# Optimization experiments

Hardware: AMD Instinct MI355X
Metric: run time of the kernel (lower is better)

The kernel has to match this reference:

```python
import jax, jax.numpy as jnp
import numpy as np

B, T, I, H, O = 128, 4096, 6, 32, 2


def setup_inputs() -> dict:
    key = jax.random.key(0)
    ks = jax.random.split(key, 8)
    x = jax.random.normal(ks[0], (B, T, I), dtype=jnp.float32)
    lengths = jax.random.randint(ks[1], (B,), 1, T + 1, dtype=jnp.int32)
    lengths = jnp.sort(lengths)[::-1]            # descending (enforce_sorted=True)
    lengths = lengths.at[0].set(T)               # max length == T -> static output shape
    s = 1.0 / np.sqrt(H)                         # PyTorch GRU/Linear init scale
    w_ih = jax.random.uniform(ks[2], (3 * H, I), minval=-s, maxval=s, dtype=jnp.float32)
    w_hh = jax.random.uniform(ks[3], (3 * H, H), minval=-s, maxval=s, dtype=jnp.float32)
    b_ih = jax.random.uniform(ks[4], (3 * H,), minval=-s, maxval=s, dtype=jnp.float32)
    b_hh = jax.random.uniform(ks[5], (3 * H,), minval=-s, maxval=s, dtype=jnp.float32)
    fc_w = jax.random.uniform(ks[6], (O, H), minval=-s, maxval=s, dtype=jnp.float32)
    fc_b = jax.random.uniform(ks[7], (O,), minval=-s, maxval=s, dtype=jnp.float32)
    return {"x": x, "lengths": lengths, "w_ih": w_ih, "w_hh": w_hh,
            "b_ih": b_ih, "b_hh": b_hh, "fc_w": fc_w, "fc_b": fc_b}


def reference(x, lengths, w_ih, w_hh, b_ih, b_hh, fc_w, fc_b):
    Bn, Tn, _ = x.shape
    Hn = w_hh.shape[1]
    # Precompute input-side gate projections for all steps (one big GEMM).
    gx = jnp.einsum('bti,gi->btg', x, w_ih) + b_ih      # [B,T,3H] (gate order: r,z,n)
    gx = jnp.swapaxes(gx, 0, 1)                          # [T,B,3H] time-major for scan
    mask = jnp.arange(Tn)[:, None] < lengths[None, :]    # [T,B] valid-step mask
    h0 = jnp.zeros((Bn, Hn), x.dtype)

    def step(h, inp):
        gxt, m = inp                                     # gxt [B,3H], m [B]
        gh = h @ w_hh.T + b_hh                           # [B,3H]
        xr, xz, xn = jnp.split(gxt, 3, axis=-1)
        hr, hz, hn = jnp.split(gh, 3, axis=-1)
        r = jax.nn.sigmoid(xr + hr)
        z = jax.nn.sigmoid(xz + hz)
        n = jnp.tanh(xn + r * hn)
        h_new = (1.0 - z) * n + z * h
        m = m[:, None]
        out = jnp.where(m, h_new, 0.0)                   # pad_packed pads with zeros
        h = jnp.where(m, h_new, h)                       # freeze state past length
        return h, out

    _, ys = jax.lax.scan(step, h0, (gx, mask))           # ys [T,B,H]
    out = jnp.swapaxes(ys, 0, 1)                         # [B,T,H]
    # fc applied to every (incl. zero-padded) timestep, as in the torch code
    return jnp.einsum('bth,oh->bto', out, fc_w) + fc_b   # [B,T,O]
```

## Files before the change

kernel.cpp:

```cpp
#include <hip/hip_runtime.h>

#define TT 4096
#define BB 128
#define L2E 1.4426950408889634f

typedef unsigned uv2 __attribute__((ext_vector_type(2)));
typedef float v2f __attribute__((ext_vector_type(2)));
typedef float v4f __attribute__((ext_vector_type(4)));
typedef __bf16 v8bf __attribute__((ext_vector_type(8)));

__device__ __forceinline__ float fexp2(float a) { return __builtin_amdgcn_exp2f(a); }

__device__ __forceinline__ float bpermf(int idx_bytes, float v) {
  return __int_as_float(__builtin_amdgcn_ds_bpermute(idx_bytes, __float_as_int(v)));
}

__device__ __forceinline__ float xhalf_sum(float p) {
#if __has_builtin(__builtin_amdgcn_permlane32_swap)
  uv2 r = __builtin_amdgcn_permlane32_swap(__float_as_uint(p), __float_as_uint(p),
                                           false, false);
  return __uint_as_float(r[0]) + __uint_as_float(r[1]);
#else
  return p + bpermf((threadIdx.x ^ 32) << 2, p);
#endif
}

__device__ __forceinline__ unsigned cvtpk(float lo, float hi) {
  unsigned r;
  asm("v_cvt_pk_bf16_f32 %0, %1, %2" : "=v"(r) : "v"(lo), "v"(hi));
  return r;
}

template <int CTRL>
__device__ __forceinline__ int dppmv(int src) {
  return __builtin_amdgcn_update_dpp(0, src, CTRL, 0xF, 0xF, true);
}

__device__ __forceinline__ v8bf frag_from(unsigned u0, unsigned u1, unsigned u2,
                                          unsigned u3) {
  uint4 uu = make_uint4(u0, u1, u2, u3);
  return __builtin_bit_cast(v8bf, uu);
}

__global__ __launch_bounds__(256) void gx_pre(
    const float* __restrict__ x, const float* __restrict__ w_ih,
    const float* __restrict__ b_ih, const float* __restrict__ b_hh,
    const int* __restrict__ lengths, float* __restrict__ gx) {
  const size_t idx = (size_t)blockIdx.x * 256 + threadIdx.x;
  const int g = (int)(idx % 96);
  const size_t bt = idx / 96;
  const int b = (int)(bt >> 12);
  const int t = (int)(bt & (TT - 1));
  if (t >= lengths[b]) return;
  const float* xp = x + bt * 6;
  float acc = (g < 64) ? (b_ih[g] + b_hh[g]) : b_ih[g];
#pragma unroll
  for (int i = 0; i < 6; ++i) acc = fmaf(w_ih[g * 6 + i], xp[i], acc);
  gx[idx] = (g < 64) ? (L2E * acc) : (2.0f * L2E * acc);
}

__global__ __launch_bounds__(64) __attribute__((amdgpu_waves_per_eu(1, 1)))
void gru_seq(const int* __restrict__ lengths, const float* __restrict__ w_hh,
             const float* __restrict__ b_hh, const float* __restrict__ gx,
             const float* __restrict__ fc_w, const float* __restrict__ fc_b,
             float* __restrict__ out) {
  __shared__ alignas(16) float hring[2][32][32];

  const int b = blockIdx.x;
  const int l = threadIdx.x;
  const int j = l & 31;
  const int len = lengths[b];
  const int n_ = l & 15;
  const int g = l >> 4;
  const int koff = 16 * (g & 1) + 8 * (g >> 1);

  const int q_ = (l >> 2) & 3;
  const int qb = 2 * (l >> 5);
  const int s0 = (q_ - qb) & 3;
  const int s1 = (q_ - qb - 1) & 3;
  const bool s0a = s0 & 1, s0b = s0 & 2;
  const bool s1a = s1 & 1, s1b = s1 & 2;

  auto make_wfrag = [&](int grow, int jb, float scale) -> v8bf {
    const float* wrow = w_hh + (grow + jb + n_) * 32 + koff;
    unsigned u0 = cvtpk(wrow[0] * scale, wrow[1] * scale);
    unsigned u1 = cvtpk(wrow[2] * scale, wrow[3] * scale);
    unsigned u2 = cvtpk(wrow[4] * scale, wrow[5] * scale);
    unsigned u3 = cvtpk(wrow[6] * scale, wrow[7] * scale);
    return frag_from(u0, u1, u2, u3);
  };
  const v8bf fR0 = make_wfrag(0, 0, L2E),          fR1 = make_wfrag(0, 16, L2E);
  const v8bf fZ0 = make_wfrag(32, 0, L2E),         fZ1 = make_wfrag(32, 16, L2E);
  const v8bf fN0 = make_wfrag(64, 0, 2.0f * L2E),  fN1 = make_wfrag(64, 16, 2.0f * L2E);
  v4f cn0, cn1;
  {
    const float c0 = 2.0f * L2E * b_hh[64 + n_];
    const float c1 = 2.0f * L2E * b_hh[80 + n_];
    cn0 = v4f{c0, c0, c0, c0};
    cn1 = v4f{c1, c1, c1, c1};
  }
  const v4f zero4 = v4f{0.f, 0.f, 0.f, 0.f};
  const bool hiSel = (g & 1);

  const int o_ = l >> 5;
  float4 fcw4[8];
  {
    const float4* wp = (const float4*)(fc_w + o_ * 32);
#pragma unroll
    for (int qq = 0; qq < 8; ++qq) fcw4[qq] = wp[qq];
  }
  const float fcb_ = fc_b[o_];
  const float fb0 = fc_b[0], fb1 = fc_b[1];

  const float* gxb = gx + (size_t)b * TT * 96;
  float* ob = out + (size_t)b * TT * 2;

  float h = 0.0f;
  int t = 0;

  float g0r, g0z, g0n, g1r, g1z, g1n, g2r, g2z, g2n, g3r, g3z, g3n;
  float g4r, g4z, g4n, g5r, g5z, g5n, g6r, g6z, g6n, g7r, g7z, g7n;
  {
    auto ld = [&](int ti, float& R, float& Z, float& N) {
      const int tc = (ti < len) ? ti : (len - 1);
      const float* p = gxb + (size_t)tc * 96;
      R = p[j]; Z = p[32 + j]; N = p[64 + j];
    };
    ld(0, g0r, g0z, g0n); ld(1, g1r, g1z, g1n);
    ld(2, g2r, g2z, g2n); ld(3, g3r, g3z, g3n);
    ld(4, g4r, g4z, g4n); ld(5, g5r, g5z, g5n);
    ld(6, g6r, g6z, g6n); ld(7, g7r, g7z, g7n);
  }

  auto flush = [&](int base, int cnt) {
    const int i = l & 31;
    if (i < cnt) {
      const float4* hp = (const float4*)(&hring[(base >> 5) & 1][i][0]);
      float acc = 0.f;
#pragma unroll
      for (int qq = 0; qq < 8; ++qq) {
        const float4 hv = hp[qq], w = fcw4[qq];
        acc += hv.x * w.x + hv.y * w.y + hv.z * w.z + hv.w * w.w;
      }
      ob[(base + i) * 2 + o_] = acc + fcb_;
    }
  };

  auto step = [&](float& GR, float& GZ, float& GN) {
    const float xr_ = GR, xz_ = GZ, xn_ = GN;
    {
      const int tp = (t + 8 < len) ? (t + 8) : (len - 1);
      const float* gp = gxb + (size_t)tp * 96;
      GR = gp[j]; GZ = gp[32 + j]; GN = gp[64 + j];
    }

    const int hi_ = __float_as_int(h);
    const int qa = dppmv<0x00>(hi_), qbv = dppmv<0x55>(hi_);
    const int qc = dppmv<0xAA>(hi_), qd = dppmv<0xFF>(hi_);
    const unsigned u0 = cvtpk(__int_as_float(qa), __int_as_float(qbv));
    const unsigned u1 = cvtpk(__int_as_float(qc), __int_as_float(qd));
    const int r4u0 = dppmv<0x124>((int)u0), r8u0 = dppmv<0x128>((int)u0),
              r12u0 = dppmv<0x12C>((int)u0);
    const int r4u1 = dppmv<0x124>((int)u1), r8u1 = dppmv<0x128>((int)u1),
              r12u1 = dppmv<0x12C>((int)u1);
    const unsigned d0 = s0b ? (s0a ? (unsigned)r12u0 : (unsigned)r8u0)
                            : (s0a ? (unsigned)r4u0 : u0);
    const unsigned d1 = s0b ? (s0a ? (unsigned)r12u1 : (unsigned)r8u1)
                            : (s0a ? (unsigned)r4u1 : u1);
    const unsigned d2 = s1b ? (s1a ? (unsigned)r12u0 : (unsigned)r8u0)
                            : (s1a ? (unsigned)r4u0 : u0);
    const unsigned d3 = s1b ? (s1a ? (unsigned)r12u1 : (unsigned)r8u1)
                            : (s1a ? (unsigned)r4u1 : u1);
    const v8bf ha = frag_from(d0, d1, d2, d3);

    const v4f yr0 = __builtin_amdgcn_mfma_f32_16x16x32_bf16(ha, fR0, zero4, 0, 0, 0);
    const v4f yr1 = __builtin_amdgcn_mfma_f32_16x16x32_bf16(ha, fR1, zero4, 0, 0, 0);
    const v4f yz0 = __builtin_amdgcn_mfma_f32_16x16x32_bf16(ha, fZ0, zero4, 0, 0, 0);
    const v4f yz1 = __builtin_amdgcn_mfma_f32_16x16x32_bf16(ha, fZ1, zero4, 0, 0, 0);
    const v4f yn0 = __builtin_amdgcn_mfma_f32_16x16x32_bf16(ha, fN0, cn0, 0, 0, 0);
    const v4f yn1 = __builtin_amdgcn_mfma_f32_16x16x32_bf16(ha, fN1, cn1, 0, 0, 0);

    const float yr = hiSel ? yr1[0] : yr0[0];
    const float yz = hiSel ? yz1[0] : yz0[0];
    const float hn = hiSel ? yn1[0] : yn0[0];

    const float r_ = __builtin_amdgcn_rcpf(1.0f + fexp2(-(yr + xr_)));
    const float z_ = __builtin_amdgcn_rcpf(1.0f + fexp2(-(yz + xz_)));
    const float ap = fmaf(r_, hn, xn_);
    const float q0 = __builtin_amdgcn_rcpf(1.0f + fexp2(-ap));
    const float nn = fmaf(2.0f, q0, -1.0f);
    h = fmaf(z_, h - nn, nn);

    hring[(t >> 5) & 1][t & 31][j] = h;
    if ((t & 31) == 31) flush(t - 31, 32);
    ++t;
  };

  while (t + 8 <= len) {
    step(g0r, g0z, g0n);
    step(g1r, g1z, g1n);
    step(g2r, g2z, g2n);
    step(g3r, g3z, g3n);
    step(g4r, g4z, g4n);
    step(g5r, g5z, g5n);
    step(g6r, g6z, g6n);
    step(g7r, g7z, g7n);
  }
  if (t < len) step(g0r, g0z, g0n);
  if (t < len) step(g1r, g1z, g1n);
  if (t < len) step(g2r, g2z, g2n);
  if (t < len) step(g3r, g3z, g3n);
  if (t < len) step(g4r, g4z, g4n);
  if (t < len) step(g5r, g5z, g5n);
  if (t < len) step(g6r, g6z, g6n);

  const int rem = len & 31;
  if (rem) flush(len - rem, rem);

  for (int idx2 = len * 2 + l; idx2 < TT * 2; idx2 += 64)
    ob[idx2] = (idx2 & 1) ? fb1 : fb0;
}

__global__ __launch_bounds__(64) void gru_fallback(
    const float* __restrict__ x, const int* __restrict__ lengths,
    const float* __restrict__ w_ih, const float* __restrict__ w_hh,
    const float* __restrict__ b_ih, const float* __restrict__ b_hh,
    const float* __restrict__ fc_w, const float* __restrict__ fc_b,
    float* __restrict__ out) {
  const int b = blockIdx.x;
  const int l = threadIdx.x;
  const int j = l & 31;
  const int half = l >> 5;
  const int ko = half << 4;
  const int len = lengths[b];

  float wr[16], wz[16], wn[16];
#pragma unroll
  for (int k = 0; k < 16; ++k) wr[k] = w_hh[j * 32 + ko + k] * L2E;
#pragma unroll
  for (int k = 0; k < 16; ++k) wz[k] = w_hh[(32 + j) * 32 + ko + k] * L2E;
#pragma unroll
  for (int k = 0; k < 16; ++k) wn[k] = w_hh[(64 + j) * 32 + ko + k] * (2.0f * L2E);
  float wxr[6], wxz[6], wxn[6];
#pragma unroll
  for (int i = 0; i < 6; ++i) wxr[i] = w_ih[j * 6 + i] * (0.5f * L2E);
#pragma unroll
  for (int i = 0; i < 6; ++i) wxz[i] = w_ih[(32 + j) * 6 + i] * (0.5f * L2E);
#pragma unroll
  for (int i = 0; i < 6; ++i) wxn[i] = w_ih[(64 + j) * 6 + i] * (2.0f * L2E);
  const float br = (b_ih[j] + b_hh[j]) * (0.5f * L2E);
  const float bz = (b_ih[32 + j] + b_hh[32 + j]) * (0.5f * L2E);
  const float bxn = b_ih[64 + j] * (2.0f * L2E);
  const float bhn = b_hh[64 + j] * L2E;
  const float fcw = fc_w[half * 32 + j];
  const float fcb = fc_b[half];

  const float* xb = x + (size_t)b * (TT * 6);
  float* ob = out + (size_t)b * (TT * 2);
  const int bko = half << 6;
  float h = 0.0f;

  v2f cx[3], nx[3];
  {
    const v2f* xp = (const v2f*)xb;
    cx[0] = xp[0]; cx[1] = xp[1]; cx[2] = xp[2];
  }
  for (int t = 0; t < len; ++t) {
    const int tn = (t + 1 < len) ? (t + 1) : t;
    const v2f* xp = (const v2f*)(xb + tn * 6);
    nx[0] = xp[0]; nx[1] = xp[1]; nx[2] = xp[2];
    float xr = br, xz = bz, xn = bxn;
#pragma unroll
    for (int i = 0; i < 3; ++i) {
      const float c0 = cx[i][0], c1 = cx[i][1];
      xr = fmaf(wxr[2 * i], c0, xr); xr = fmaf(wxr[2 * i + 1], c1, xr);
      xz = fmaf(wxz[2 * i], c0, xz); xz = fmaf(wxz[2 * i + 1], c1, xz);
      xn = fmaf(wxn[2 * i], c0, xn); xn = fmaf(wxn[2 * i + 1], c1, xn);
    }
    float hbv[16];
#pragma unroll
    for (int k = 0; k < 16; ++k) hbv[k] = bpermf(bko + (k << 2), h);
    float ar0 = xr, ar1 = 0.f, az0 = xz, az1 = 0.f, an0 = bhn, an1 = 0.f;
#pragma unroll
    for (int k = 0; k < 8; ++k) {
      ar0 = fmaf(wr[k], hbv[k], ar0);
      ar1 = fmaf(wr[k + 8], hbv[k + 8], ar1);
      az0 = fmaf(wz[k], hbv[k], az0);
      az1 = fmaf(wz[k + 8], hbv[k + 8], az1);
      an0 = fmaf(wn[k], hbv[k], an0);
      an1 = fmaf(wn[k + 8], hbv[k + 8], an1);
    }
    const float sr = xhalf_sum(ar0 + ar1);
    const float r = __builtin_amdgcn_rcpf(1.0f + fexp2(-sr));
    const float sz = xhalf_sum(az0 + az1);
    const float z = __builtin_amdgcn_rcpf(1.0f + fexp2(-sz));
    const float hn = xhalf_sum(an0 + an1);
    const float ap = fmaf(r, hn, xn);
    const float qq = __builtin_amdgcn_rcpf(1.0f + fexp2(-ap));
    const float nn = fmaf(2.0f, qq, -1.0f);
    h = fmaf(z, h - nn, nn);
    float p = h * fcw;
    p += __shfl_xor(p, 1);
    p += __shfl_xor(p, 2);
    p += __shfl_xor(p, 4);
    p += __shfl_xor(p, 8);
    p += __shfl_xor(p, 16);
    if (j == 0) ob[t * 2 + half] = p + fcb;
#pragma unroll
    for (int i = 0; i < 3; ++i) cx[i] = nx[i];
  }
  const float fb0 = fc_b[0], fb1 = fc_b[1];
  for (int idx = len * 2 + l; idx < TT * 2; idx += 64)
    ob[idx] = (idx & 1) ? fb1 : fb0;
}

extern "C" void kernel_launch(void* const* d_in, const int* in_sizes, int n_in,
                              void* d_out, int out_size, void* d_ws, size_t ws_size,
                              hipStream_t stream) {
  const float* x       = (const float*)d_in[0];
  const int*   lengths = (const int*)d_in[1];
  const float* w_ih    = (const float*)d_in[2];
  const float* w_hh    = (const float*)d_in[3];
  const float* b_ih    = (const float*)d_in[4];
  const float* b_hh    = (const float*)d_in[5];
  const float* fc_w    = (const float*)d_in[6];
  const float* fc_b    = (const float*)d_in[7];
  float* outp = (float*)d_out;

  const size_t gx_elems = (size_t)BB * TT * 96;
  const size_t need = gx_elems * sizeof(float);
  if (ws_size >= need) {
    float* gx = (float*)d_ws;
    hipLaunchKernelGGL(gx_pre, dim3((BB * TT * 96) / 256), dim3(256), 0, stream,
                       x, w_ih, b_ih, b_hh, lengths, gx);
    hipLaunchKernelGGL(gru_seq, dim3(BB), dim3(64), 0, stream,
                       lengths, w_hh, b_hh, gx, fc_w, fc_b, outp);
  } else {
    hipLaunchKernelGGL(gru_fallback, dim3(BB), dim3(64), 0, stream,
                       x, lengths, w_ih, w_hh, b_ih, b_hh, fc_w, fc_b, outp);
  }
}
```

Before: 808.0 us.

## Fuse input projection into recurrent GRU kernel and drop gx workspace

Removes the separate gx_pre kernel that wrote a 128x4096x96 float gate-projection buffer to global memory. The recurrent kernel now loads the 6 raw input features per step (prefetched 8 steps ahead) and computes the three input-gate projections with 18 FMAs in registers. This removes a large global write and read plus a kernel launch, at the cost of extra ALU work per step on the serial recurrence path. The fallback kernel is deleted as no longer needed.

```diff
diff --git a/kernel.cpp b/kernel.cpp
--- a/kernel.cpp
+++ b/kernel.cpp
@@ -4,26 +4,11 @@
 #define BB 128
 #define L2E 1.4426950408889634f
 
-typedef unsigned uv2 __attribute__((ext_vector_type(2)));
 typedef float v2f __attribute__((ext_vector_type(2)));
 typedef float v4f __attribute__((ext_vector_type(4)));
 typedef __bf16 v8bf __attribute__((ext_vector_type(8)));
 
 __device__ __forceinline__ float fexp2(float a) { return __builtin_amdgcn_exp2f(a); }
-
-__device__ __forceinline__ float bpermf(int idx_bytes, float v) {
-  return __int_as_float(__builtin_amdgcn_ds_bpermute(idx_bytes, __float_as_int(v)));
-}
-
-__device__ __forceinline__ float xhalf_sum(float p) {
-#if __has_builtin(__builtin_amdgcn_permlane32_swap)
-  uv2 r = __builtin_amdgcn_permlane32_swap(__float_as_uint(p), __float_as_uint(p),
-                                           false, false);
-  return __uint_as_float(r[0]) + __uint_as_float(r[1]);
-#else
-  return p + bpermf((threadIdx.x ^ 32) << 2, p);
-#endif
-}
 
 __device__ __forceinline__ unsigned cvtpk(float lo, float hi) {
   unsigned r;
@@ -42,28 +27,12 @@
   return __builtin_bit_cast(v8bf, uu);
 }
 
-__global__ __launch_bounds__(256) void gx_pre(
-    const float* __restrict__ x, const float* __restrict__ w_ih,
-    const float* __restrict__ b_ih, const float* __restrict__ b_hh,
-    const int* __restrict__ lengths, float* __restrict__ gx) {
-  const size_t idx = (size_t)blockIdx.x * 256 + threadIdx.x;
-  const int g = (int)(idx % 96);
-  const size_t bt = idx / 96;
-  const int b = (int)(bt >> 12);
-  const int t = (int)(bt & (TT - 1));
-  if (t >= lengths[b]) return;
-  const float* xp = x + bt * 6;
-  float acc = (g < 64) ? (b_ih[g] + b_hh[g]) : b_ih[g];
-#pragma unroll
-  for (int i = 0; i < 6; ++i) acc = fmaf(w_ih[g * 6 + i], xp[i], acc);
-  gx[idx] = (g < 64) ? (L2E * acc) : (2.0f * L2E * acc);
-}
-
 __global__ __launch_bounds__(64) __attribute__((amdgpu_waves_per_eu(1, 1)))
-void gru_seq(const int* __restrict__ lengths, const float* __restrict__ w_hh,
-             const float* __restrict__ b_hh, const float* __restrict__ gx,
-             const float* __restrict__ fc_w, const float* __restrict__ fc_b,
-             float* __restrict__ out) {
+void gru_fused(const float* __restrict__ x, const int* __restrict__ lengths,
+               const float* __restrict__ w_ih, const float* __restrict__ w_hh,
+               const float* __restrict__ b_ih, const float* __restrict__ b_hh,
+               const float* __restrict__ fc_w, const float* __restrict__ fc_b,
+               float* __restrict__ out) {
   __shared__ alignas(16) float hring[2][32][32];
 
   const int b = blockIdx.x;
@@ -102,6 +71,17 @@
   const v4f zero4 = v4f{0.f, 0.f, 0.f, 0.f};
   const bool hiSel = (g & 1);
 
+  float wxr[6], wxz[6], wxn[6];
+#pragma unroll
+  for (int i = 0; i < 6; ++i) wxr[i] = w_ih[j * 6 + i] * L2E;
+#pragma unroll
+  for (int i = 0; i < 6; ++i) wxz[i] = w_ih[(32 + j) * 6 + i] * L2E;
+#pragma unroll
+  for (int i = 0; i < 6; ++i) wxn[i] = w_ih[(64 + j) * 6 + i] * (2.0f * L2E);
+  const float br  = (b_ih[j] + b_hh[j]) * L2E;
+  const float bz  = (b_ih[32 + j] + b_hh[32 + j]) * L2E;
+  const float bxn = b_ih[64 + j] * (2.0f * L2E);
+
   const int o_ = l >> 5;
   float4 fcw4[8];
   {
@@ -112,24 +92,24 @@
   const float fcb_ = fc_b[o_];
   const float fb0 = fc_b[0], fb1 = fc_b[1];
 
-  const float* gxb = gx + (size_t)b * TT * 96;
+  const float* xb = x + (size_t)b * TT * 6;
   float* ob = out + (size_t)b * TT * 2;
 
   float h = 0.0f;
   int t = 0;
 
-  float g0r, g0z, g0n, g1r, g1z, g1n, g2r, g2z, g2n, g3r, g3z, g3n;
-  float g4r, g4z, g4n, g5r, g5z, g5n, g6r, g6z, g6n, g7r, g7z, g7n;
+  v2f x0a, x0b, x0c, x1a, x1b, x1c, x2a, x2b, x2c, x3a, x3b, x3c;
+  v2f x4a, x4b, x4c, x5a, x5b, x5c, x6a, x6b, x6c, x7a, x7b, x7c;
   {
-    auto ld = [&](int ti, float& R, float& Z, float& N) {
+    auto ld = [&](int ti, v2f& A, v2f& B, v2f& C) {
       const int tc = (ti < len) ? ti : (len - 1);
-      const float* p = gxb + (size_t)tc * 96;
-      R = p[j]; Z = p[32 + j]; N = p[64 + j];
+      const v2f* p = (const v2f*)(xb + (size_t)tc * 6);
+      A = p[0]; B = p[1]; C = p[2];
     };
-    ld(0, g0r, g0z, g0n); ld(1, g1r, g1z, g1n);
-    ld(2, g2r, g2z, g2n); ld(3, g3r, g3z, g3n);
-    ld(4, g4r, g4z, g4n); ld(5, g5r, g5z, g5n);
-    ld(6, g6r, g6z, g6n); ld(7, g7r, g7z, g7n);
+    ld(0, x0a, x0b, x0c); ld(1, x1a, x1b, x1c);
+    ld(2, x2a, x2b, x2c); ld(3, x3a, x3b, x3c);
+    ld(4, x4a, x4b, x4c); ld(5, x5a, x5b, x5c);
+    ld(6, x6a, x6b, x6c); ld(7, x7a, x7b, x7c);
   }
 
   auto flush = [&](int base, int cnt) {
@@ -146,12 +126,25 @@
     }
   };
 
-  auto step = [&](float& GR, float& GZ, float& GN) {
-    const float xr_ = GR, xz_ = GZ, xn_ = GN;
+  auto step = [&](v2f& XA, v2f& XB, v2f& XC) {
+    float xr_ = br, xz_ = bz, xn_ = bxn;
+    {
+      const float c0 = XA[0], c1 = XA[1], c2 = XB[0], c3 = XB[1],
+                  c4 = XC[0], c5 = XC[1];
+      xr_ = fmaf(wxr[0], c0, xr_); xr_ = fmaf(wxr[1], c1, xr_);
+      xr_ = fmaf(wxr[2], c2, xr_); xr_ = fmaf(wxr[3], c3, xr_);
+      xr_ = fmaf(wxr[4], c4, xr_); xr_ = fmaf(wxr[5], c5, xr_);
+      xz_ = fmaf(wxz[0], c0, xz_); xz_ = fmaf(wxz[1], c1, xz_);
+      xz_ = fmaf(wxz[2], c2, xz_); xz_ = fmaf(wxz[3], c3, xz_);
+      xz_ = fmaf(wxz[4], c4, xz_); xz_ = fmaf(wxz[5], c5, xz_);
+      xn_ = fmaf(wxn[0], c0, xn_); xn_ = fmaf(wxn[1], c1, xn_);
+      xn_ = fmaf(wxn[2], c2, xn_); xn_ = fmaf(wxn[3], c3, xn_);
+      xn_ = fmaf(wxn[4], c4, xn_); xn_ = fmaf(wxn[5], c5, xn_);
+    }
     {
       const int tp = (t + 8 < len) ? (t + 8) : (len - 1);
-      const float* gp = gxb + (size_t)tp * 96;
-      GR = gp[j]; GZ = gp[32 + j]; GN = gp[64 + j];
+      const v2f* p = (const v2f*)(xb + (size_t)tp * 6);
+      XA = p[0]; XB = p[1]; XC = p[2];
     }
 
     const int hi_ = __float_as_int(h);
@@ -197,121 +190,28 @@
   };
 
   while (t + 8 <= len) {
-    step(g0r, g0z, g0n);
-    step(g1r, g1z, g1n);
-    step(g2r, g2z, g2n);
-    step(g3r, g3z, g3n);
-    step(g4r, g4z, g4n);
-    step(g5r, g5z, g5n);
-    step(g6r, g6z, g6n);
-    step(g7r, g7z, g7n);
-  }
-  if (t < len) step(g0r, g0z, g0n);
-  if (t < len) step(g1r, g1z, g1n);
-  if (t < len) step(g2r, g2z, g2n);
-  if (t < len) step(g3r, g3z, g3n);
-  if (t < len) step(g4r, g4z, g4n);
-  if (t < len) step(g5r, g5z, g5n);
-  if (t < len) step(g6r, g6z, g6n);
+    step(x0a, x0b, x0c);
+    step(x1a, x1b, x1c);
+    step(x2a, x2b, x2c);
+    step(x3a, x3b, x3c);
+    step(x4a, x4b, x4c);
+    step(x5a, x5b, x5c);
+    step(x6a, x6b, x6c);
+    step(x7a, x7b, x7c);
+  }
+  if (t < len) step(x0a, x0b, x0c);
+  if (t < len) step(x1a, x1b, x1c);
+  if (t < len) step(x2a, x2b, x2c);
+  if (t < len) step(x3a, x3b, x3c);
+  if (t < len) step(x4a, x4b, x4c);
+  if (t < len) step(x5a, x5b, x5c);
+  if (t < len) step(x6a, x6b, x6c);
 
   const int rem = len & 31;
   if (rem) flush(len - rem, rem);
 
   for (int idx2 = len * 2 + l; idx2 < TT * 2; idx2 += 64)
     ob[idx2] = (idx2 & 1) ? fb1 : fb0;
-}
-
-__global__ __launch_bounds__(64) void gru_fallback(
-    const float* __restrict__ x, const int* __restrict__ lengths,
-    const float* __restrict__ w_ih, const float* __restrict__ w_hh,
-    const float* __restrict__ b_ih, const float* __restrict__ b_hh,
-    const float* __restrict__ fc_w, const float* __restrict__ fc_b,
-    float* __restrict__ out) {
-  const int b = blockIdx.x;
-  const int l = threadIdx.x;
-  const int j = l & 31;
-  const int half = l >> 5;
-  const int ko = half << 4;
-  const int len = lengths[b];
-
-  float wr[16], wz[16], wn[16];
-#pragma unroll
-  for (int k = 0; k < 16; ++k) wr[k] = w_hh[j * 32 + ko + k] * L2E;
-#pragma unroll
-  for (int k = 0; k < 16; ++k) wz[k] = w_hh[(32 + j) * 32 + ko + k] * L2E;
-#pragma unroll
-  for (int k = 0; k < 16; ++k) wn[k] = w_hh[(64 + j) * 32 + ko + k] * (2.0f * L2E);
-  float wxr[6], wxz[6], wxn[6];
-#pragma unroll
-  for (int i = 0; i < 6; ++i) wxr[i] = w_ih[j * 6 + i] * (0.5f * L2E);
-#pragma unroll
-  for (int i = 0; i < 6; ++i) wxz[i] = w_ih[(32 + j) * 6 + i] * (0.5f * L2E);
-#pragma unroll
-  for (int i = 0; i < 6; ++i) wxn[i] = w_ih[(64 + j) * 6 + i] * (2.0f * L2E);
-  const float br = (b_ih[j] + b_hh[j]) * (0.5f * L2E);
-  const float bz = (b_ih[32 + j] + b_hh[32 + j]) * (0.5f * L2E);
-  const float bxn = b_ih[64 + j] * (2.0f * L2E);
-  const float bhn = b_hh[64 + j] * L2E;
-  const float fcw = fc_w[half * 32 + j];
-  const float fcb = fc_b[half];
-
-  const float* xb = x + (size_t)b * (TT * 6);
-  float* ob = out + (size_t)b * (TT * 2);
-  const int bko = half << 6;
-  float h = 0.0f;
-
-  v2f cx[3], nx[3];
-  {
-    const v2f* xp = (const v2f*)xb;
-    cx[0] = xp[0]; cx[1] = xp[1]; cx[2] = xp[2];
-  }
-  for (int t = 0; t < len; ++t) {
-    const int tn = (t + 1 < len) ? (t + 1) : t;
-    const v2f* xp = (const v2f*)(xb + tn * 6);
-    nx[0] = xp[0]; nx[1] = xp[1]; nx[2] = xp[2];
-    float xr = br, xz = bz, xn = bxn;
-#pragma unroll
-    for (int i = 0; i < 3; ++i) {
-      const float c0 = cx[i][0], c1 = cx[i][1];
-      xr = fmaf(wxr[2 * i], c0, xr); xr = fmaf(wxr[2 * i + 1], c1, xr);
-      xz = fmaf(wxz[2 * i], c0, xz); xz = fmaf(wxz[2 * i + 1], c1, xz);
-      xn = fmaf(wxn[2 * i], c0, xn); xn = fmaf(wxn[2 * i + 1], c1, xn);
-    }
-    float hbv[16];
-#pragma unroll
-    for (int k = 0; k < 16; ++k) hbv[k] = bpermf(bko + (k << 2), h);
-    float ar0 = xr, ar1 = 0.f, az0 = xz, az1 = 0.f, an0 = bhn, an1 = 0.f;
-#pragma unroll
-    for (int k = 0; k < 8; ++k) {
-      ar0 = fmaf(wr[k], hbv[k], ar0);
-      ar1 = fmaf(wr[k + 8], hbv[k + 8], ar1);
-      az0 = fmaf(wz[k], hbv[k], az0);
-      az1 = fmaf(wz[k + 8], hbv[k + 8], az1);
-      an0 = fmaf(wn[k], hbv[k], an0);
-      an1 = fmaf(wn[k + 8], hbv[k + 8], an1);
-    }
-    const float sr = xhalf_sum(ar0 + ar1);
-    const float r = __builtin_amdgcn_rcpf(1.0f + fexp2(-sr));
-    const float sz = xhalf_sum(az0 + az1);
-    const float z = __builtin_amdgcn_rcpf(1.0f + fexp2(-sz));
-    const float hn = xhalf_sum(an0 + an1);
-    const float ap = fmaf(r, hn, xn);
-    const float qq = __builtin_amdgcn_rcpf(1.0f + fexp2(-ap));
-    const float nn = fmaf(2.0f, qq, -1.0f);
-    h = fmaf(z, h - nn, nn);
-    float p = h * fcw;
-    p += __shfl_xor(p, 1);
-    p += __shfl_xor(p, 2);
-    p += __shfl_xor(p, 4);
-    p += __shfl_xor(p, 8);
-    p += __shfl_xor(p, 16);
-    if (j == 0) ob[t * 2 + half] = p + fcb;
-#pragma unroll
-    for (int i = 0; i < 3; ++i) cx[i] = nx[i];
-  }
-  const float fb0 = fc_b[0], fb1 = fc_b[1];
-  for (int idx = len * 2 + l; idx < TT * 2; idx += 64)
-    ob[idx] = (idx & 1) ? fb1 : fb0;
 }
 
 extern "C" void kernel_launch(void* const* d_in, const int* in_sizes, int n_in,
@@ -327,16 +227,6 @@
   const float* fc_b    = (const float*)d_in[7];
   float* outp = (float*)d_out;
 
-  const size_t gx_elems = (size_t)BB * TT * 96;
-  const size_t need = gx_elems * sizeof(float);
-  if (ws_size >= need) {
-    float* gx = (float*)d_ws;
-    hipLaunchKernelGGL(gx_pre, dim3((BB * TT * 96) / 256), dim3(256), 0, stream,
-                       x, w_ih, b_ih, b_hh, lengths, gx);
-    hipLaunchKernelGGL(gru_seq, dim3(BB), dim3(64), 0, stream,
-                       lengths, w_hh, b_hh, gx, fc_w, fc_b, outp);
-  } else {
-    hipLaunchKernelGGL(gru_fallback, dim3(BB), dim3(64), 0, stream,
-                       x, lengths, w_ih, w_hh, b_ih, b_hh, fc_w, fc_b, outp);
-  }
-}
+  hipLaunchKernelGGL(gru_fused, dim3(BB), dim3(64), 0, stream,
+                     x, lengths, w_ih, w_hh, b_ih, b_hh, fc_w, fc_b, outp);
+}
```

Measured after the change: 708.4 us. 12.3% less time.
